# Optimization experiments

Hardware: AMD Instinct MI355X
Metric: run time of the kernel (lower is better)

The kernel has to match this reference:

```python
import jax, jax.numpy as jnp
import numpy as np

B, H, S, D = 1, 16, 4096, 64

def setup_inputs() -> dict:
    key = jax.random.key(0)
    kq, kk, kv = jax.random.split(key, 3)
    q = jax.random.normal(kq, (B, H, S, D), dtype=jnp.float32)
    k = jax.random.normal(kk, (B, H, D, S), dtype=jnp.float32)  # pre-transposed, as in torch forward
    v = jax.random.normal(kv, (B, H, S, D), dtype=jnp.float32)
    return {"q": q, "k": k, "v": v}

def reference(q, k, v):
    # w = q @ k  -> [B, H, S, S]
    w = jnp.einsum('bhsd,bhdt->bhst', q, k)
    w = w / jnp.sqrt(jnp.asarray(v.shape[-1], w.dtype))
    # causal mask applied exactly as the original: w*b + -1e9*(1-b)
    s_q, s_k = w.shape[-2], w.shape[-1]
    b = jnp.tril(jnp.ones((s_q, s_k), dtype=w.dtype))[None, None]
    w = w * b + (-1e9) * (1.0 - b)
    w = jax.nn.softmax(w, axis=-1)
    # dropout p=0.0 -> identity
    return jnp.einsum('bhst,bhtd->bhsd', w, v)
```

## Files before the change

### kernel.cpp

```cpp
#include <hip/hip_runtime.h>
#include <hip/hip_bf16.h>
#include <math.h>

typedef __bf16 bf16_t;
typedef __bf16 bf16x4 __attribute__((ext_vector_type(4)));
typedef __bf16 bf16x8 __attribute__((ext_vector_type(8)));
typedef float  f32x4  __attribute__((ext_vector_type(4)));

static constexpr int S_LEN = 4096;
static constexpr int D_DIM = 64;
static constexpr int H_NUM = 16;
static constexpr int BT    = 64;
static constexpr float QSCALE = 0.18033688011112042f;
static constexpr float MB2    = 12.0f;

__device__ __forceinline__ float fexp2(float x) {
#if __has_builtin(__builtin_amdgcn_exp2f)
  return __builtin_amdgcn_exp2f(x);
#else
  return exp2f(x);
#endif
}

__global__ __launch_bounds__(256)
void prepack(const float* __restrict__ kg, const float* __restrict__ vg,
             bf16_t* __restrict__ ktr, bf16_t* __restrict__ vq) {
  __shared__ bf16_t tk[64][72];
  __shared__ bf16_t tv[64][72];
  const int tid = threadIdx.x;
  const int h = blockIdx.x >> 6, sb = blockIdx.x & 63;
  const int s0 = sb * 64;
  const float* kh = kg + (size_t)h * D_DIM * S_LEN;
  const float* vh = vg + (size_t)h * S_LEN * D_DIM;

  #pragma unroll
  for (int it = 0; it < 4; ++it) {
    const int d = (tid >> 4) + it * 16;
    const int s = (tid & 15) * 4;
    const f32x4 x = *(const f32x4*)(kh + (size_t)d * S_LEN + s0 + s);
    #pragma unroll
    for (int i = 0; i < 4; ++i) tk[s + i][d] = (bf16_t)x[i];
    const f32x4 y = *(const f32x4*)(vh + (size_t)(s0 + d) * D_DIM + s);
    bf16x4 yb;
    #pragma unroll
    for (int i = 0; i < 4; ++i) yb[i] = (bf16_t)y[i];
    *(bf16x4*)&tv[d][s] = yb;
  }
  __syncthreads();

  {
    const int s = tid >> 2, c = (tid & 3) * 16;
    const bf16x8 a = *(const bf16x8*)&tk[s][c];
    const bf16x8 b = *(const bf16x8*)&tk[s][c + 8];
    bf16_t* o = ktr + ((size_t)h * S_LEN + s0 + s) * D_DIM + c;
    *(bf16x8*)o = a;
    *(bf16x8*)(o + 8) = b;
  }
  {
    const int f  = tid >> 5;
    const int kt = f >> 2, nt = f & 3;
    const int l0 = (tid & 31) * 2;
    #pragma unroll
    for (int li = 0; li < 2; ++li) {
      const int l = l0 + li;
      const int colv = l & 15, quadv = l >> 4;
      const int d = nt * 16 + colv;
      bf16x8 w;
      #pragma unroll
      for (int j = 0; j < 8; ++j) {
        const int t = kt * 32 + (j >> 2) * 16 + quadv * 4 + (j & 3);
        w[j] = tv[t][d];
      }
      *(bf16x8*)(vq + (((size_t)(h * 64 + sb) * 8 + f) * 512 + l * 8)) = w;
    }
  }
}

__global__ __launch_bounds__(256, 4)
void attn_fwd(const float* __restrict__ qg, const bf16_t* __restrict__ ktr,
              const bf16_t* __restrict__ vq, float* __restrict__ og) {
  __shared__ __align__(16) bf16_t kT[2][64][72];

  const int tid  = threadIdx.x;
  const int wave = tid >> 6;
  const int lane = tid & 63;
  const int col  = lane & 15;
  const int quad = lane >> 4;

  const int h = blockIdx.x & 15;
  const int p = blockIdx.x >> 4;

  const float*  qh  = qg  + (size_t)h * S_LEN * D_DIM;
  const bf16_t* kth = ktr + (size_t)h * S_LEN * D_DIM;
  const bf16_t* vqh = vq  + (size_t)h * 64 * 8 * 512;
  float*        oh  = og  + (size_t)h * S_LEN * D_DIM;

  const int st = tid >> 2;
  const int sc = (tid & 3) * 16;

  const bf16_t* vbase = vqh + (size_t)lane * 8;

  for (int ph = 0; ph < 2; ++ph) {
    const int qt = ph ? (63 - p) : p;
    const int qbase = qt * 64;
    const int wr0 = qbase + wave * 16;
    const int nsteps = qt + 1;

    bf16x8 qb[2];
    {
      const float* qp = qh + (size_t)(wr0 + col) * D_DIM;
      #pragma unroll
      for (int kk = 0; kk < 2; ++kk) {
        f32x4 lo = *(const f32x4*)(qp + kk * 32 + quad * 8);
        f32x4 hi = *(const f32x4*)(qp + kk * 32 + quad * 8 + 4);
        #pragma unroll
        for (int j = 0; j < 4; ++j) {
          qb[kk][j]     = (bf16_t)(lo[j] * QSCALE);
          qb[kk][j + 4] = (bf16_t)(hi[j] * QSCALE);
        }
      }
    }

    f32x4 acc[4];
    #pragma unroll
    for (int nt = 0; nt < 4; ++nt) acc[nt] = (f32x4){0.f, 0.f, 0.f, 0.f};
    float l_i = 0.f;

    {
      const bf16_t* kp = kth + (size_t)st * 64 + sc;
      *(bf16x8*)&kT[0][st][sc]     = *(const bf16x8*)kp;
      *(bf16x8*)&kT[0][st][sc + 8] = *(const bf16x8*)(kp + 8);
    }
    __syncthreads();

    for (int s = 0; s < nsteps; ++s) {
      const int buf = s & 1;
      const int t0  = s * BT;
      const bool pf = (s + 1 < nsteps);

      bf16x8 kf[4][2];
      #pragma unroll
      for (int ct = 0; ct < 4; ++ct)
        #pragma unroll
        for (int kk = 0; kk < 2; ++kk)
          kf[ct][kk] = *(const bf16x8*)&kT[buf][ct * 16 + col][kk * 32 + quad * 8];

      const bf16_t* vb = vbase + (size_t)s * 4096;
      const bf16x8 vf00 = *(const bf16x8*)(vb);
      const bf16x8 vf01 = *(const bf16x8*)(vb + 512);
      const bf16x8 vf02 = *(const bf16x8*)(vb + 1024);
      const bf16x8 vf03 = *(const bf16x8*)(vb + 1536);
      const bf16x8 vf10 = *(const bf16x8*)(vb + 2048);
      const bf16x8 vf11 = *(const bf16x8*)(vb + 2560);
      const bf16x8 vf12 = *(const bf16x8*)(vb + 3072);
      const bf16x8 vf13 = *(const bf16x8*)(vb + 3584);

      bf16x8 kp0, kp1;
      if (pf) {
        const bf16_t* kp = kth + (size_t)(t0 + BT + st) * 64 + sc;
        kp0 = *(const bf16x8*)kp;
        kp1 = *(const bf16x8*)(kp + 8);
      }

      f32x4 sc_[4];
      #pragma unroll
      for (int ct = 0; ct < 4; ++ct) sc_[ct] = (f32x4){-MB2, -MB2, -MB2, -MB2};
      __builtin_amdgcn_s_setprio(1);
      #pragma unroll
      for (int ct = 0; ct < 4; ++ct)
        #pragma unroll
        for (int kk = 0; kk < 2; ++kk)
          sc_[ct] = __builtin_amdgcn_mfma_f32_16x16x32_bf16(kf[ct][kk], qb[kk], sc_[ct], 0, 0, 0);
      __builtin_amdgcn_s_setprio(0);

      bf16x8 pfrag[2];
      {
        const int qrow = wr0 + col;
        if (t0 + BT - 1 > wr0) {
          #pragma unroll
          for (int ct = 0; ct < 4; ++ct)
            #pragma unroll
            for (int r = 0; r < 4; ++r)
              sc_[ct][r] = (t0 + ct * 16 + quad * 4 + r > qrow) ? -1e30f : sc_[ct][r];
        }
        float rs0 = 0.f, rs1 = 0.f;
        #pragma unroll
        for (int ct = 0; ct < 4; ++ct) {
          const float p0 = fexp2(sc_[ct][0]);
          const float p1 = fexp2(sc_[ct][1]);
          const float p2 = fexp2(sc_[ct][2]);
          const float p3 = fexp2(sc_[ct][3]);
          rs0 += p0 + p1; rs1 += p2 + p3;
          const int kt = ct >> 1, hh = (ct & 1) * 4;
          pfrag[kt][hh + 0] = (bf16_t)p0;
          pfrag[kt][hh + 1] = (bf16_t)p1;
          pfrag[kt][hh + 2] = (bf16_t)p2;
          pfrag[kt][hh + 3] = (bf16_t)p3;
        }
        l_i += rs0 + rs1;
      }

      if (pf) {
        *(bf16x8*)&kT[buf ^ 1][st][sc]     = kp0;
        *(bf16x8*)&kT[buf ^ 1][st][sc + 8] = kp1;
      }

      __builtin_amdgcn_s_setprio(1);
      acc[0] = __builtin_amdgcn_mfma_f32_16x16x32_bf16(vf00, pfrag[0], acc[0], 0, 0, 0);
      acc[1] = __builtin_amdgcn_mfma_f32_16x16x32_bf16(vf01, pfrag[0], acc[1], 0, 0, 0);
      acc[2] = __builtin_amdgcn_mfma_f32_16x16x32_bf16(vf02, pfrag[0], acc[2], 0, 0, 0);
      acc[3] = __builtin_amdgcn_mfma_f32_16x16x32_bf16(vf03, pfrag[0], acc[3], 0, 0, 0);
      acc[0] = __builtin_amdgcn_mfma_f32_16x16x32_bf16(vf10, pfrag[1], acc[0], 0, 0, 0);
      acc[1] = __builtin_amdgcn_mfma_f32_16x16x32_bf16(vf11, pfrag[1], acc[1], 0, 0, 0);
      acc[2] = __builtin_amdgcn_mfma_f32_16x16x32_bf16(vf12, pfrag[1], acc[2], 0, 0, 0);
      acc[3] = __builtin_amdgcn_mfma_f32_16x16x32_bf16(vf13, pfrag[1], acc[3], 0, 0, 0);
      __builtin_amdgcn_s_setprio(0);

      __syncthreads();
    }

    {
      float l = l_i;
      l += __shfl_xor(l, 16);
      l += __shfl_xor(l, 32);
      const float inv_l = 1.0f / l;
      const int qr = wr0 + col;
      float* op = oh + (size_t)qr * D_DIM + quad * 4;
      #pragma unroll
      for (int nt = 0; nt < 4; ++nt) {
        f32x4 o;
        o[0] = acc[nt][0] * inv_l; o[1] = acc[nt][1] * inv_l;
        o[2] = acc[nt][2] * inv_l; o[3] = acc[nt][3] * inv_l;
        *(f32x4*)(op + nt * 16) = o;
      }
    }
  }
}

extern "C" void kernel_launch(void* const* d_in, const int* in_sizes, int n_in,
                              void* d_out, int out_size, void* d_ws, size_t ws_size,
                              hipStream_t stream) {
  const float* q = (const float*)d_in[0];
  const float* k = (const float*)d_in[1];
  const float* v = (const float*)d_in[2];
  float* out = (float*)d_out;

  const size_t KB = (size_t)H_NUM * S_LEN * D_DIM * 2;
  bf16_t* ktr = (bf16_t*)d_ws;
  bf16_t* vq  = (bf16_t*)((char*)d_ws + KB);

  dim3 block(256);
  prepack<<<dim3(H_NUM * 64), block, 0, stream>>>(k, v, ktr, vq);
  attn_fwd<<<dim3(H_NUM * 32), block, 0, stream>>>(q, ktr, vq, out);
}
```

Measured before the change: 150.1 us.

## Split each paired causal block across two wave groups with KV-split reduction

Each block grows to 512 threads in two 256-thread subgroups that run concurrently instead of processing the two paired query tiles in sequence. Subgroup 0 handles the short tile p and then the first part of tile 63-p's KV range, while subgroup 1 handles the rest, so both take 32 or 33 steps. Partial accumulators and row sums are merged through shared memory before the final normalisation, which is valid because the kernel uses a fixed max offset rather than a running max. The aim is to halve the serial per-block length and raise wave-level parallelism, at the cost of doubled LDS per block and block-wide barriers shared by both subgroups.

```diff
diff --git a/kernel.cpp b/kernel.cpp
--- a/kernel.cpp
+++ b/kernel.cpp
@@ -76,13 +76,14 @@
   }
 }
 
-__global__ __launch_bounds__(256, 4)
+__global__ __launch_bounds__(512, 4)
 void attn_fwd(const float* __restrict__ qg, const bf16_t* __restrict__ ktr,
               const bf16_t* __restrict__ vq, float* __restrict__ og) {
-  __shared__ __align__(16) bf16_t kT[2][64][72];
+  __shared__ __align__(16) bf16_t kTs[2][2][64][72];
 
   const int tid  = threadIdx.x;
-  const int wave = tid >> 6;
+  const int sid  = tid >> 8;
+  const int w4   = (tid >> 6) & 3;
   const int lane = tid & 63;
   const int col  = lane & 15;
   const int quad = lane >> 4;
@@ -95,57 +96,64 @@
   const bf16_t* vqh = vq  + (size_t)h * 64 * 8 * 512;
   float*        oh  = og  + (size_t)h * S_LEN * D_DIM;
 
-  const int st = tid >> 2;
-  const int sc = (tid & 3) * 16;
+  const int qtB = 63 - p;
+  const int nmy = sid ? 33 : 32;
+
+  bf16_t* kTb = &kTs[sid][0][0][0];
+
+  const int stid = tid & 255;
+  const int st   = stid >> 2;
+  const int scc  = (stid & 3) * 16;
 
   const bf16_t* vbase = vqh + (size_t)lane * 8;
 
-  for (int ph = 0; ph < 2; ++ph) {
-    const int qt = ph ? (63 - p) : p;
-    const int qbase = qt * 64;
-    const int wr0 = qbase + wave * 16;
-    const int nsteps = qt + 1;
-
-    bf16x8 qb[2];
-    {
-      const float* qp = qh + (size_t)(wr0 + col) * D_DIM;
-      #pragma unroll
-      for (int kk = 0; kk < 2; ++kk) {
-        f32x4 lo = *(const f32x4*)(qp + kk * 32 + quad * 8);
-        f32x4 hi = *(const f32x4*)(qp + kk * 32 + quad * 8 + 4);
-        #pragma unroll
-        for (int j = 0; j < 4; ++j) {
-          qb[kk][j]     = (bf16_t)(lo[j] * QSCALE);
-          qb[kk][j + 4] = (bf16_t)(hi[j] * QSCALE);
-        }
-      }
-    }
-
-    f32x4 acc[4];
-    #pragma unroll
-    for (int nt = 0; nt < 4; ++nt) acc[nt] = (f32x4){0.f, 0.f, 0.f, 0.f};
-    float l_i = 0.f;
-
-    {
-      const bf16_t* kp = kth + (size_t)st * 64 + sc;
-      *(bf16x8*)&kT[0][st][sc]     = *(const bf16x8*)kp;
-      *(bf16x8*)&kT[0][st][sc + 8] = *(const bf16x8*)(kp + 8);
-    }
-    __syncthreads();
-
-    for (int s = 0; s < nsteps; ++s) {
-      const int buf = s & 1;
-      const int t0  = s * BT;
-      const bool pf = (s + 1 < nsteps);
-
+  int wr0 = (sid ? qtB : p) * 64 + w4 * 16;
+
+  bf16x8 qb[2];
+  {
+    const float* qp = qh + (size_t)(wr0 + col) * D_DIM;
+    #pragma unroll
+    for (int kk = 0; kk < 2; ++kk) {
+      f32x4 lo = *(const f32x4*)(qp + kk * 32 + quad * 8);
+      f32x4 hi = *(const f32x4*)(qp + kk * 32 + quad * 8 + 4);
+      #pragma unroll
+      for (int j = 0; j < 4; ++j) {
+        qb[kk][j]     = (bf16_t)(lo[j] * QSCALE);
+        qb[kk][j + 4] = (bf16_t)(hi[j] * QSCALE);
+      }
+    }
+  }
+
+  f32x4 acc[4];
+  #pragma unroll
+  for (int nt = 0; nt < 4; ++nt) acc[nt] = (f32x4){0.f, 0.f, 0.f, 0.f};
+  float l_i = 0.f;
+
+  {
+    const int kv0 = sid ? (31 - p) : 0;
+    const bf16_t* kp = kth + (size_t)(kv0 * 64 + st) * 64 + scc;
+    *(bf16x8*)(kTb + st * 72 + scc)     = *(const bf16x8*)kp;
+    *(bf16x8*)(kTb + st * 72 + scc + 8) = *(const bf16x8*)(kp + 8);
+  }
+  __syncthreads();
+
+  for (int i = 0; i < 33; ++i) {
+    if (i < nmy) {
+      const int kv  = sid ? (31 - p + i) : ((i <= p) ? i : (i - p - 1));
+      const int kvn = sid ? (31 - p + i + 1) : ((i + 1 <= p) ? (i + 1) : (i - p));
+      const int buf = i & 1;
+      const bool pf = (i + 1 < nmy);
+      const int t0  = kv * BT;
+
+      const bf16_t* kb = kTb + buf * 4608;
       bf16x8 kf[4][2];
       #pragma unroll
       for (int ct = 0; ct < 4; ++ct)
         #pragma unroll
         for (int kk = 0; kk < 2; ++kk)
-          kf[ct][kk] = *(const bf16x8*)&kT[buf][ct * 16 + col][kk * 32 + quad * 8];
-
-      const bf16_t* vb = vbase + (size_t)s * 4096;
+          kf[ct][kk] = *(const bf16x8*)(kb + (ct * 16 + col) * 72 + kk * 32 + quad * 8);
+
+      const bf16_t* vb = vbase + (size_t)kv * 4096;
       const bf16x8 vf00 = *(const bf16x8*)(vb);
       const bf16x8 vf01 = *(const bf16x8*)(vb + 512);
       const bf16x8 vf02 = *(const bf16x8*)(vb + 1024);
@@ -157,7 +165,7 @@
 
       bf16x8 kp0, kp1;
       if (pf) {
-        const bf16_t* kp = kth + (size_t)(t0 + BT + st) * 64 + sc;
+        const bf16_t* kp = kth + (size_t)(kvn * 64 + st) * 64 + scc;
         kp0 = *(const bf16x8*)kp;
         kp1 = *(const bf16x8*)(kp + 8);
       }
@@ -201,8 +209,8 @@
       }
 
       if (pf) {
-        *(bf16x8*)&kT[buf ^ 1][st][sc]     = kp0;
-        *(bf16x8*)&kT[buf ^ 1][st][sc + 8] = kp1;
+        *(bf16x8*)(kTb + (buf ^ 1) * 4608 + st * 72 + scc)     = kp0;
+        *(bf16x8*)(kTb + (buf ^ 1) * 4608 + st * 72 + scc + 8) = kp1;
       }
 
       __builtin_amdgcn_s_setprio(1);
@@ -216,23 +224,71 @@
       acc[3] = __builtin_amdgcn_mfma_f32_16x16x32_bf16(vf13, pfrag[1], acc[3], 0, 0, 0);
       __builtin_amdgcn_s_setprio(0);
 
-      __syncthreads();
-    }
-
-    {
-      float l = l_i;
-      l += __shfl_xor(l, 16);
-      l += __shfl_xor(l, 32);
-      const float inv_l = 1.0f / l;
-      const int qr = wr0 + col;
-      float* op = oh + (size_t)qr * D_DIM + quad * 4;
-      #pragma unroll
-      for (int nt = 0; nt < 4; ++nt) {
-        f32x4 o;
-        o[0] = acc[nt][0] * inv_l; o[1] = acc[nt][1] * inv_l;
-        o[2] = acc[nt][2] * inv_l; o[3] = acc[nt][3] * inv_l;
-        *(f32x4*)(op + nt * 16) = o;
-      }
+      if (sid == 0 && i == p) {
+        float l = l_i;
+        l += __shfl_xor(l, 16);
+        l += __shfl_xor(l, 32);
+        const float inv_l = 1.0f / l;
+        float* op = oh + (size_t)(wr0 + col) * D_DIM + quad * 4;
+        #pragma unroll
+        for (int nt = 0; nt < 4; ++nt) {
+          f32x4 o;
+          o[0] = acc[nt][0] * inv_l; o[1] = acc[nt][1] * inv_l;
+          o[2] = acc[nt][2] * inv_l; o[3] = acc[nt][3] * inv_l;
+          *(f32x4*)(op + nt * 16) = o;
+        }
+        if (p < 31) {
+          #pragma unroll
+          for (int nt = 0; nt < 4; ++nt) acc[nt] = (f32x4){0.f, 0.f, 0.f, 0.f};
+          l_i = 0.f;
+          wr0 = qtB * 64 + w4 * 16;
+          const float* qp = qh + (size_t)(wr0 + col) * D_DIM;
+          #pragma unroll
+          for (int kk = 0; kk < 2; ++kk) {
+            f32x4 lo = *(const f32x4*)(qp + kk * 32 + quad * 8);
+            f32x4 hi = *(const f32x4*)(qp + kk * 32 + quad * 8 + 4);
+            #pragma unroll
+            for (int j = 0; j < 4; ++j) {
+              qb[kk][j]     = (bf16_t)(lo[j] * QSCALE);
+              qb[kk][j + 4] = (bf16_t)(hi[j] * QSCALE);
+            }
+          }
+        }
+      }
+    }
+    __syncthreads();
+  }
+
+  if (sid == 0 && p < 31) {
+    float* cb = (float*)&kTs[0][0][0][0] + (size_t)(w4 * 64 + lane) * 17;
+    #pragma unroll
+    for (int nt = 0; nt < 4; ++nt)
+      #pragma unroll
+      for (int r = 0; r < 4; ++r) cb[nt * 4 + r] = acc[nt][r];
+    cb[16] = l_i;
+  }
+  __syncthreads();
+
+  if (sid == 1) {
+    if (p < 31) {
+      const float* cb = (const float*)&kTs[0][0][0][0] + (size_t)(w4 * 64 + lane) * 17;
+      #pragma unroll
+      for (int nt = 0; nt < 4; ++nt)
+        #pragma unroll
+        for (int r = 0; r < 4; ++r) acc[nt][r] += cb[nt * 4 + r];
+      l_i += cb[16];
+    }
+    float l = l_i;
+    l += __shfl_xor(l, 16);
+    l += __shfl_xor(l, 32);
+    const float inv_l = 1.0f / l;
+    float* op = oh + (size_t)(wr0 + col) * D_DIM + quad * 4;
+    #pragma unroll
+    for (int nt = 0; nt < 4; ++nt) {
+      f32x4 o;
+      o[0] = acc[nt][0] * inv_l; o[1] = acc[nt][1] * inv_l;
+      o[2] = acc[nt][2] * inv_l; o[3] = acc[nt][3] * inv_l;
+      *(f32x4*)(op + nt * 16) = o;
     }
   }
 }
@@ -249,7 +305,6 @@
   bf16_t* ktr = (bf16_t*)d_ws;
   bf16_t* vq  = (bf16_t*)((char*)d_ws + KB);
 
-  dim3 block(256);
-  prepack<<<dim3(H_NUM * 64), block, 0, stream>>>(k, v, ktr, vq);
-  attn_fwd<<<dim3(H_NUM * 32), block, 0, stream>>>(q, ktr, vq, out);
+  prepack<<<dim3(H_NUM * 64), dim3(256), 0, stream>>>(k, v, ktr, vq);
+  attn_fwd<<<dim3(H_NUM * 32), dim3(512), 0, stream>>>(q, ktr, vq, out);
 }
```

Measured after the change: 149.8 us. No clear change (-0.2%).
